# Kernel tuning notes

Measured on AMD Instinct MI355X. Metric: run time of the kernel, lower is better.

Reference implementation:

```python
import jax, jax.numpy as jnp
import numpy as np
import math

EPS = 1e-5
NEG_SLOPE = 0.2

def _patches(x, k=3, s=2):
    # x: (N, C, H, W) -> (N, C, k*k, Ho, Wo); VALID padding, stride s
    N, C = x.shape[0], x.shape[1]
    p = jax.lax.conv_general_dilated_patches(x, (k, k), (s, s), 'VALID')
    return p.reshape(N, C, k * k, p.shape[2], p.shape[3])

def _pacconv(x, guide, w, b, k=3):
    # PacConv2d (gaussian kernel, smooth_kernel_type='none', no normalization)
    xp = _patches(x)                              # (N,Cin,K2,Ho,Wo)
    gp = _patches(guide)                          # (N,Cg,K2,Ho,Wo)
    ctr = (k * k) // 2
    d = gp - gp[:, :, ctr:ctr + 1]
    ker = jnp.exp(-0.5 * jnp.sum(d * d, axis=1, keepdims=True))  # (N,1,K2,Ho,Wo)
    out = jnp.einsum('nckhw,ock->nohw', xp * ker,
                     w.reshape(w.shape[0], w.shape[1], k * k))
    return out + b[None, :, None, None]

def _conv(x, w, b):
    out = jax.lax.conv_general_dilated(x, w, (2, 2), 'VALID',
                                       dimension_numbers=('NCHW', 'OIHW', 'NCHW'))
    return out + b[None, :, None, None]

def _avgpool(x):
    s = jax.lax.reduce_window(x, 0.0, jax.lax.add, (1, 1, 3, 3), (1, 1, 2, 2), 'VALID')
    return s / 9.0

def _lrelu(x):
    return jnp.where(x >= 0, x, NEG_SLOPE * x)

def _bn(x, g, b):
    # training-mode BatchNorm2d (batch stats, biased variance)
    m = jnp.mean(x, axis=(0, 2, 3), keepdims=True)
    v = jnp.mean((x - m) ** 2, axis=(0, 2, 3), keepdims=True)
    xn = (x - m) * jax.lax.rsqrt(v + EPS)
    return xn * g[None, :, None, None] + b[None, :, None, None]

def setup_inputs() -> dict:
    key = jax.random.key(0)
    ks = jax.random.split(key, 12)
    N, Cin, H = 128, 1, 120
    x = jax.random.normal(ks[0], (N, Cin, H, H), jnp.float32)
    guide = jax.random.uniform(ks[1], (N, 1, H, H), jnp.float32)
    def wconv(k, co, ci):
        return jax.random.normal(k, (co, ci, 3, 3), jnp.float32) * (1.0 / math.sqrt(ci * 9))
    w1, b1 = wconv(ks[2], 32, Cin), jnp.zeros((32,), jnp.float32)
    w2, b2 = wconv(ks[3], 64, 32), jnp.zeros((64,), jnp.float32)
    w3, b3 = wconv(ks[4], 128, 64), jnp.zeros((128,), jnp.float32)
    w4, b4 = wconv(ks[5], 256, 128), jnp.zeros((256,), jnp.float32)
    g2, be2 = jnp.ones((64,), jnp.float32), jnp.zeros((64,), jnp.float32)
    g3, be3 = jnp.ones((128,), jnp.float32), jnp.zeros((128,), jnp.float32)
    g4, be4 = jnp.ones((256,), jnp.float32), jnp.zeros((256,), jnp.float32)
    wadv = jax.random.normal(ks[6], (1, 9216), jnp.float32)  # EqualLinear raw weight
    badv = jnp.ones((1,), jnp.float32)                        # bias_init=1
    return {"x": x, "guide": guide, "w1": w1, "b1": b1, "w2": w2, "b2": b2,
            "w3": w3, "b3": b3, "w4": w4, "b4": b4, "g2": g2, "be2": be2,
            "g3": g3, "be3": be3, "g4": g4, "be4": be4, "wadv": wadv, "badv": badv}

def reference(x, guide, w1, b1, w2, b2, w3, b3, w4, b4,
              g2, be2, g3, be3, g4, be4, wadv, badv):
    out = _lrelu(_conv(x, w1, b1))                 # (N,32,59,59)
    guide = _avgpool(guide)                        # (N,1,59,59)
    out = _bn(_lrelu(_pacconv(out, guide, w2, b2)), g2, be2)   # (N,64,29,29)
    guide = _avgpool(guide)                        # (N,1,29,29)
    out = _bn(_lrelu(_pacconv(out, guide, w3, b3)), g3, be3)   # (N,128,14,14)
    guide = _avgpool(guide)                        # (N,1,14,14)
    out = _bn(_lrelu(_pacconv(out, guide, w4, b4)), g4, be4)   # (N,256,6,6)
    flat = out.reshape(out.shape[0], -1)           # (N,9216)
    scale = 1.0 / math.sqrt(9216)
    validity = flat @ (wadv * scale).T + badv      # EqualLinear, lr_mul=1
    return validity
```

## Files before the change

kernel.cpp:

```cpp
#include <hip/hip_runtime.h>
#include <hip/hip_bf16.h>

#define EPSBN 1e-5f
#define NEG_SLOPE 0.2f

using f32x4  = __attribute__((ext_vector_type(4))) float;
using bf16x8 = __attribute__((ext_vector_type(8))) short;

#define O_Y1B     0
#define O_G1      7129088
#define O_Y2B     7574656
#define O_G2      11019392
#define O_WKB2    11127040
#define O_WKB3    11136256
#define O_WKB4    11173120
#define O_WADVR   11320576
#define O_ACC     11329792
#define O_G3      11336960
#define O_Y3B     11362048
#define O_POUT4   12967680
#define O_Y4      16506624
#define A_ACC2    0
#define A_ACC3    1024
#define A_ACC4    3072

__device__ __forceinline__ unsigned short f2bf(float f) {
  union { float f; unsigned int u; } v; v.f = f;
  unsigned int u = v.u + 0x7FFF + ((v.u >> 16) & 1);
  return (unsigned short)(u >> 16);
}
__device__ __forceinline__ float bf2f(unsigned short u) {
  union { unsigned int i; float f; } x; x.i = (unsigned int)u << 16; return x.f;
}

#define CONV1_B 7552
#define AVG1_B  1741
#define RPK_B   1548
#define ZERO_B  7
__global__ __launch_bounds__(256) void prep_kernel(
    const float* __restrict__ x, const float* __restrict__ gd,
    const float* __restrict__ w1, const float* __restrict__ b1,
    const float* __restrict__ w2, const float* __restrict__ w3,
    const float* __restrict__ w4, const float* __restrict__ wadv,
    float* __restrict__ ws) {
  const int bi = blockIdx.x, tid = threadIdx.x;
  __shared__ float xs[360];
  __shared__ float wsm[320];
  if (bi < CONV1_B) {
    const int n = bi / 59, oh = bi % 59;
    for (int i = tid; i < 320; i += 256)
      wsm[i] = (i < 288) ? w1[(i & 31) * 9 + (i >> 5)] : b1[i - 288];
    const float* src = x + ((size_t)n * 120 + oh * 2) * 120;
    for (int i = tid; i < 360; i += 256) xs[i] = src[i];
    __syncthreads();
    const int co = tid & 31;
    const int ow0 = (tid >> 5) * 8;
    float w[9];
#pragma unroll
    for (int k = 0; k < 9; ++k) w[k] = wsm[k * 32 + co];
    const float bias = wsm[288 + co];
    unsigned short* yb = (unsigned short*)(ws + O_Y1B) + (size_t)(n * 59 + oh) * 59 * 32;
#pragma unroll
    for (int j = 0; j < 8; ++j) {
      int ow = ow0 + j;
      if (ow < 59) {
        float acc = bias;
#pragma unroll
        for (int kh = 0; kh < 3; ++kh)
#pragma unroll
          for (int kw = 0; kw < 3; ++kw)
            acc += xs[kh * 120 + ow * 2 + kw] * w[kh * 3 + kw];
        acc = acc >= 0.0f ? acc : NEG_SLOPE * acc;
        yb[ow * 32 + co] = f2bf(acc);
      }
    }
  } else if (bi < CONV1_B + AVG1_B) {
    int idx = (bi - CONV1_B) * 256 + tid;
    if (idx < 445568) {
      int ow = idx % 59; int t = idx / 59; int oh = t % 59; int n = t / 59;
      const float* gb = gd + (n * 120 + oh * 2) * 120 + ow * 2;
      float s = 0.0f;
#pragma unroll
      for (int kh = 0; kh < 3; ++kh)
#pragma unroll
        for (int kw = 0; kw < 3; ++kw) s += gb[kh * 120 + kw];
      ws[O_G1 + idx] = s * (1.0f / 9.0f);
    }
  } else if (bi < CONV1_B + AVG1_B + RPK_B) {
    int idx = (bi - CONV1_B - AVG1_B) * 256 + tid;
    if (idx < 18432) {
      int kk = idx & 31; int t = idx >> 5; int co = t & 63; int tap = t >> 6;
      ((unsigned short*)(ws + O_WKB2))[idx] = f2bf(w2[(co * 32 + kk) * 9 + tap]);
    } else if (idx < 92160) {
      int i = idx - 18432;
      int kk = i & 31; int t = i >> 5; int co = t & 127; int t3 = t >> 7;
      int kc = t3 & 1; int tap = t3 >> 1;
      ((unsigned short*)(ws + O_WKB3))[i] = f2bf(w3[(co * 64 + kc * 32 + kk) * 9 + tap]);
    } else if (idx < 387072) {
      int i = idx - 92160;
      int kk = i & 31; int t = i >> 5; int co = t & 255; int t3 = t >> 8;
      int kc = t3 & 3; int tap = t3 >> 2;
      ((unsigned short*)(ws + O_WKB4))[i] = f2bf(w4[(co * 128 + kc * 32 + kk) * 9 + tap]);
    } else if (idx < 396288) {
      int i = idx - 387072;
      int c = i & 255; int hw = i >> 8;
      ws[O_WADVR + i] = wadv[c * 36 + hw] * (1.0f / 96.0f);
    }
  } else {
    int idx = (bi - CONV1_B - AVG1_B - RPK_B) * 256 + tid;
    if (idx * 4 < 7168) {
      float4 z = {0.0f, 0.0f, 0.0f, 0.0f};
      *reinterpret_cast<float4*>(ws + O_ACC + idx * 4) = z;
    }
  }
}

template <int CI, int CO, int HI, int HO, int NWM, int NWN, bool BN_IN,
          bool FUSE, int SSEG, int NBLK, int MINW, bool POOL>
__global__ __launch_bounds__(256, MINW)
void pac_kernel(const unsigned short* __restrict__ xb, const float* __restrict__ g,
                const float* __restrict__ wkb_f, const float* __restrict__ b,
                const float* __restrict__ gamma, const float* __restrict__ beta,
                const float* __restrict__ accin, float invM,
                unsigned short* __restrict__ yb, float* __restrict__ pout,
                float* __restrict__ accout,
                const float* __restrict__ pin, float* __restrict__ pgout,
                int PHI, int PHO, int PTOT) {
  constexpr int KC   = CI / 32;
  constexpr int NSEG = (9 * KC) / SSEG;
  constexpr int TSEG = SSEG / KC;
  static_assert(SSEG % KC == 0, "tap-aligned segments");
  constexpr int MBLK = NWM * 32;
  constexpr int PIX  = NBLK * MBLK;
  constexpr int BSZ  = BN_IN ? CI : 1;
  constexpr int PSM  = FUSE ? NWM : 1;
  constexpr int PSN  = FUSE ? CO * 2 : 1;
  const unsigned short* wkb = (const unsigned short*)wkb_f;

  const int tid  = threadIdx.x;
  const int bi   = blockIdx.x;

  if constexpr (POOL) {
    if (bi >= NBLK * NSEG) {
      int idx = (bi - NBLK * NSEG) * 256 + tid;
      if (idx < PTOT) {
        int ow = idx % PHO; int t = idx / PHO; int oh = t % PHO; int n = t / PHO;
        const float* gb = pin + (n * PHI + oh * 2) * PHI + ow * 2;
        float s = 0.0f;
#pragma unroll
        for (int kh = 0; kh < 3; ++kh)
#pragma unroll
          for (int kw = 0; kw < 3; ++kw) s += gb[kh * PHI + kw];
        pgout[idx] = s * (1.0f / 9.0f);
      }
      return;
    }
  }

  __shared__ float bscl[BSZ], bshl[BSZ];
  __shared__ float ps[PSM][PSN];

  const int lane = tid & 63;
  const int wv   = tid >> 6;
  const int wm   = wv / NWN, wn = wv % NWN;
  const int kseg = bi / NBLK;
  const int blk  = bi % NBLK;
  const int s0   = kseg * SSEG;
  const int tapb = kseg * TSEG;
  const int l15  = lane & 15;
  const int g8   = (lane >> 4) * 8;

  if constexpr (BN_IN) {
    if (tid < CI) {
      float s = 0.0f, q = 0.0f;
#pragma unroll
      for (int sl = 0; sl < 8; ++sl) {
        s += accin[(sl * CI + tid) * 2 + 0];
        q += accin[(sl * CI + tid) * 2 + 1];
      }
      float m = s * invM;
      float var = q * invM - m * m;
      float sc = gamma[tid] * rsqrtf(var + EPSBN);
      bscl[tid] = sc;
      bshl[tid] = beta[tid] - m * sc;
    }
    __syncthreads();
  }

  float kk[2][TSEG];
  int   xo[2];
  int   xt[TSEG];
#pragma unroll
  for (int t = 0; t < TSEG; ++t) {
    int tap = tapb + t;
    xt[t] = ((tap / 3) * HI + (tap % 3)) * CI;
  }
#pragma unroll
  for (int mt = 0; mt < 2; ++mt) {
    int p  = blk * MBLK + wm * 32 + mt * 16 + l15;
    int ow = p % HO, oh = (p / HO) % HO, n = p / (HO * HO);
    const float* gn = g + n * (HI * HI);
    float gc = gn[(oh * 2 + 1) * HI + ow * 2 + 1];
#pragma unroll
    for (int t = 0; t < TSEG; ++t) {
      int tap = tapb + t;
      float d = gn[(oh * 2 + tap / 3) * HI + ow * 2 + (tap % 3)] - gc;
      kk[mt][t] = __expf(-0.5f * d * d);
    }
    xo[mt] = ((n * HI + oh * 2) * HI + ow * 2) * CI;
  }

  f32x4 acc[2][4];
#pragma unroll
  for (int nt = 0; nt < 4; ++nt) {
    float bv = FUSE ? b[wn * 64 + nt * 16 + l15] : 0.0f;
#pragma unroll
    for (int mt = 0; mt < 2; ++mt) acc[mt][nt] = (f32x4){bv, bv, bv, bv};
  }

#pragma unroll
  for (int i = 0; i < SSEG; ++i) {
    const int t  = i / KC;
    const int kc = i % KC;
    bf16x8 bfv[4];
#pragma unroll
    for (int nt = 0; nt < 4; ++nt)
      bfv[nt] = *(const bf16x8*)(wkb + ((size_t)(s0 + i) * CO + wn * 64 + nt * 16 + l15) * 32 + g8);
    bf16x8 af[2];
#pragma unroll
    for (int mt = 0; mt < 2; ++mt) {
      const unsigned short* ax = xb + xo[mt] + xt[t] + kc * 32 + g8;
      bf16x8 u = *(const bf16x8*)ax;
      float v[8];
#pragma unroll
      for (int j = 0; j < 8; ++j) v[j] = bf2f((unsigned short)u[j]);
      if constexpr (BN_IN) {
        const int c0 = kc * 32 + g8;
#pragma unroll
        for (int j = 0; j < 8; ++j) v[j] = v[j] * bscl[c0 + j] + bshl[c0 + j];
      }
      const float kv = kk[mt][t];
#pragma unroll
      for (int j = 0; j < 8; ++j) v[j] *= kv;
#pragma unroll
      for (int j = 0; j < 8; ++j) af[mt][j] = (short)f2bf(v[j]);
    }
#pragma unroll
    for (int mt = 0; mt < 2; ++mt)
#pragma unroll
      for (int nt = 0; nt < 4; ++nt)
        acc[mt][nt] = __builtin_amdgcn_mfma_f32_16x16x32_bf16(af[mt], bfv[nt], acc[mt][nt], 0, 0, 0);
  }

  if constexpr (FUSE) {
#pragma unroll
    for (int nt = 0; nt < 4; ++nt) {
      const int co = wn * 64 + nt * 16 + l15;
      float s = 0.0f, q = 0.0f;
#pragma unroll
      for (int mt = 0; mt < 2; ++mt)
#pragma unroll
        for (int r = 0; r < 4; ++r) {
          float v = acc[mt][nt][r];
          v = v >= 0.0f ? v : NEG_SLOPE * v;
          int p = blk * MBLK + wm * 32 + mt * 16 + ((lane >> 4) << 2) + r;
          yb[(size_t)p * CO + co] = f2bf(v);
          s += v; q += v * v;
        }
      s += __shfl_xor(s, 16, 64); q += __shfl_xor(q, 16, 64);
      s += __shfl_xor(s, 32, 64); q += __shfl_xor(q, 32, 64);
      if (l15 == lane) { ps[wm][co * 2 + 0] = s; ps[wm][co * 2 + 1] = q; }
    }
    __syncthreads();
    if (tid < CO) {
      float s = 0.0f, q = 0.0f;
#pragma unroll
      for (int wmx = 0; wmx < NWM; ++wmx) { s += ps[wmx][tid * 2]; q += ps[wmx][tid * 2 + 1]; }
      atomicAdd(&accout[((blk & 7) * CO + tid) * 2 + 0], s);
      atomicAdd(&accout[((blk & 7) * CO + tid) * 2 + 1], q);
    }
  } else {
#pragma unroll
    for (int nt = 0; nt < 4; ++nt) {
      const int co = wn * 64 + nt * 16 + l15;
#pragma unroll
      for (int mt = 0; mt < 2; ++mt)
#pragma unroll
        for (int r = 0; r < 4; ++r) {
          int p = blk * MBLK + wm * 32 + mt * 16 + ((lane >> 4) << 2) + r;
          pout[((size_t)kseg * PIX + p) * CO + co] = acc[mt][nt][r];
        }
    }
  }
}

template <int CO, int EPT, int NSEG>
__global__ void combine_kernel(const float* __restrict__ pout, int pixco,
                               const float* __restrict__ b,
                               float* __restrict__ y, float* __restrict__ acc) {
  const int tid = threadIdx.x, blk = blockIdx.x;
  const int base = blk * (256 * EPT);
  const int co = tid & (CO - 1);
  const float bias = b[co];
  float s = 0.0f, q = 0.0f;
#pragma unroll
  for (int i = 0; i < EPT; ++i) {
    int e = base + i * 256 + tid;
    float v = bias;
#pragma unroll
    for (int sg = 0; sg < NSEG; ++sg) v += pout[(size_t)sg * pixco + e];
    v = v >= 0.0f ? v : NEG_SLOPE * v;
    y[e] = v;
    s += v; q += v * v;
  }
  atomicAdd(&acc[((blk & 7) * CO + co) * 2 + 0], s);
  atomicAdd(&acc[((blk & 7) * CO + co) * 2 + 1], q);
}

__global__ void linear_kernel(const float* __restrict__ y4, const float* __restrict__ acc4,
                              const float* __restrict__ bg4, const float* __restrict__ bb4,
                              const float* __restrict__ wadvr, const float* __restrict__ badv,
                              float* __restrict__ out) {
  int n = blockIdx.x, t = threadIdx.x;
  float s0 = 0.0f, q0 = 0.0f;
#pragma unroll
  for (int sl = 0; sl < 8; ++sl) {
    s0 += acc4[(sl * 256 + t) * 2 + 0];
    q0 += acc4[(sl * 256 + t) * 2 + 1];
  }
  float m = s0 * (1.0f / 4608.0f);
  float var = q0 * (1.0f / 4608.0f) - m * m;
  float sc = bg4[t] * rsqrtf(var + EPSBN);
  float sh = bb4[t] - m * sc;
  float s = 0.0f;
  for (int j = t; j < 9216; j += 256) s += (y4[n * 9216 + j] * sc + sh) * wadvr[j];
  __shared__ float ss[256];
  ss[t] = s; __syncthreads();
  for (int off = 128; off > 0; off >>= 1) {
    if (t < off) ss[t] += ss[t + off];
    __syncthreads();
  }
  if (t == 0) out[n] = ss[0] + badv[0];
}

extern "C" void kernel_launch(void* const* d_in, const int* in_sizes, int n_in,
                              void* d_out, int out_size, void* d_ws, size_t ws_size,
                              hipStream_t stream) {
  const float* x    = (const float*)d_in[0];
  const float* gd   = (const float*)d_in[1];
  const float* w1   = (const float*)d_in[2];
  const float* b1   = (const float*)d_in[3];
  const float* w2   = (const float*)d_in[4];
  const float* b2   = (const float*)d_in[5];
  const float* w3   = (const float*)d_in[6];
  const float* b3   = (const float*)d_in[7];
  const float* w4   = (const float*)d_in[8];
  const float* b4   = (const float*)d_in[9];
  const float* bg2  = (const float*)d_in[10];
  const float* bb2  = (const float*)d_in[11];
  const float* bg3  = (const float*)d_in[12];
  const float* bb3  = (const float*)d_in[13];
  const float* bg4  = (const float*)d_in[14];
  const float* bb4  = (const float*)d_in[15];
  const float* wadv = (const float*)d_in[16];
  const float* badv = (const float*)d_in[17];
  float* out = (float*)d_out;
  float* ws  = (float*)d_ws;

  unsigned short* y1b = (unsigned short*)(ws + O_Y1B);
  unsigned short* y2b = (unsigned short*)(ws + O_Y2B);
  unsigned short* y3b = (unsigned short*)(ws + O_Y3B);
  float* acc2 = ws + O_ACC + A_ACC2;
  float* acc3 = ws + O_ACC + A_ACC3;
  float* acc4 = ws + O_ACC + A_ACC4;

  prep_kernel<<<CONV1_B + AVG1_B + RPK_B + ZERO_B, 256, 0, stream>>>(
      x, gd, w1, b1, w2, w3, w4, wadv, ws);

  pac_kernel<32, 64, 59, 29, 4, 1, false, true, 9, 841, 3, true>
      <<<1262, 256, 0, stream>>>(y1b, ws + O_G1, ws + O_WKB2, b2,
                                 nullptr, nullptr, nullptr, 0.0f,
                                 y2b, nullptr, acc2,
                                 ws + O_G1, ws + O_G2, 59, 29, 107648);

  pac_kernel<64, 128, 29, 14, 2, 2, true, true, 18, 392, 2, true>
      <<<490, 256, 0, stream>>>(y2b, ws + O_G2, ws + O_WKB3, b3,
                                bg2, bb2, acc2, 1.0f / 107648.0f,
                                y3b, nullptr, acc3,
                                ws + O_G2, ws + O_G3, 29, 14, 25088);

  pac_kernel<128, 256, 14, 6, 1, 4, true, false, 12, 144, 2, false>
      <<<432, 256, 0, stream>>>(y3b, ws + O_G3, ws + O_WKB4, nullptr,
                                bg3, bb3, acc3, 1.0f / 25088.0f,
                                nullptr, ws + O_POUT4, nullptr,
                                nullptr, nullptr, 0, 0, 0);

  combine_kernel<256, 8, 3><<<576, 256, 0, stream>>>(ws + O_POUT4, 1179648, b4,
                                                     ws + O_Y4, acc4);

  linear_kernel<<<128, 256, 0, stream>>>(ws + O_Y4, acc4, bg4, bb4,
                                         ws + O_WADVR, badv, out);
}
```

Baseline: 105.4 us.

## Drop split-K for layer 4, fuse combine into pac kernel, stage stores through LDS

Removes the split-K segmentation so each pac block computes all taps. Layer 4 now applies bias, LeakyReLU and BN statistics in-kernel and writes bf16 output, so the combine kernel and its fp32 partial-sum round trip go away. Output tiles in both conv1 and the pac kernels are staged in shared memory and written with wide coalesced stores. The catch is that layer 4 launches only 144 blocks, each with a longer serial K loop, which lowers parallelism on a large GPU. f2bf now uses the HIP intrinsic, and linear_kernel reads bf16 activations.

```diff
diff --git a/kernel.cpp b/kernel.cpp
--- a/kernel.cpp
+++ b/kernel.cpp
@@ -18,16 +18,15 @@
 #define O_ACC     11329792
 #define O_G3      11336960
 #define O_Y3B     11362048
-#define O_POUT4   12967680
-#define O_Y4      16506624
+#define O_Y4B     12967680
 #define A_ACC2    0
 #define A_ACC3    1024
 #define A_ACC4    3072
 
 __device__ __forceinline__ unsigned short f2bf(float f) {
-  union { float f; unsigned int u; } v; v.f = f;
-  unsigned int u = v.u + 0x7FFF + ((v.u >> 16) & 1);
-  return (unsigned short)(u >> 16);
+  union { __hip_bfloat16 b; unsigned short u; } cv;
+  cv.b = __float2bfloat16(f);
+  return cv.u;
 }
 __device__ __forceinline__ float bf2f(unsigned short u) {
   union { unsigned int i; float f; } x; x.i = (unsigned int)u << 16; return x.f;
@@ -46,6 +45,7 @@
   const int bi = blockIdx.x, tid = threadIdx.x;
   __shared__ float xs[360];
   __shared__ float wsm[320];
+  __shared__ unsigned short ysm[1888];
   if (bi < CONV1_B) {
     const int n = bi / 59, oh = bi % 59;
     for (int i = tid; i < 320; i += 256)
@@ -59,7 +59,6 @@
 #pragma unroll
     for (int k = 0; k < 9; ++k) w[k] = wsm[k * 32 + co];
     const float bias = wsm[288 + co];
-    unsigned short* yb = (unsigned short*)(ws + O_Y1B) + (size_t)(n * 59 + oh) * 59 * 32;
 #pragma unroll
     for (int j = 0; j < 8; ++j) {
       int ow = ow0 + j;
@@ -71,9 +70,14 @@
           for (int kw = 0; kw < 3; ++kw)
             acc += xs[kh * 120 + ow * 2 + kw] * w[kh * 3 + kw];
         acc = acc >= 0.0f ? acc : NEG_SLOPE * acc;
-        yb[ow * 32 + co] = f2bf(acc);
-      }
-    }
+        ysm[ow * 32 + co] = f2bf(acc);
+      }
+    }
+    __syncthreads();
+    unsigned int* dst = (unsigned int*)((unsigned short*)(ws + O_Y1B) +
+                                        (size_t)(n * 59 + oh) * 1888);
+    const unsigned int* s2 = (const unsigned int*)ysm;
+    for (int i = tid; i < 944; i += 256) dst[i] = s2[i];
   } else if (bi < CONV1_B + AVG1_B) {
     int idx = (bi - CONV1_B) * 256 + tid;
     if (idx < 445568) {
@@ -116,33 +120,27 @@
 }
 
 template <int CI, int CO, int HI, int HO, int NWM, int NWN, bool BN_IN,
-          bool FUSE, int SSEG, int NBLK, int MINW, bool POOL>
+          int NBLK, int MINW, bool POOL>
 __global__ __launch_bounds__(256, MINW)
 void pac_kernel(const unsigned short* __restrict__ xb, const float* __restrict__ g,
                 const float* __restrict__ wkb_f, const float* __restrict__ b,
                 const float* __restrict__ gamma, const float* __restrict__ beta,
                 const float* __restrict__ accin, float invM,
-                unsigned short* __restrict__ yb, float* __restrict__ pout,
-                float* __restrict__ accout,
+                unsigned short* __restrict__ yb, float* __restrict__ accout,
                 const float* __restrict__ pin, float* __restrict__ pgout,
                 int PHI, int PHO, int PTOT) {
   constexpr int KC   = CI / 32;
-  constexpr int NSEG = (9 * KC) / SSEG;
-  constexpr int TSEG = SSEG / KC;
-  static_assert(SSEG % KC == 0, "tap-aligned segments");
+  constexpr int S    = 9 * KC;
   constexpr int MBLK = NWM * 32;
-  constexpr int PIX  = NBLK * MBLK;
   constexpr int BSZ  = BN_IN ? CI : 1;
-  constexpr int PSM  = FUSE ? NWM : 1;
-  constexpr int PSN  = FUSE ? CO * 2 : 1;
   const unsigned short* wkb = (const unsigned short*)wkb_f;
 
-  const int tid  = threadIdx.x;
-  const int bi   = blockIdx.x;
+  const int tid = threadIdx.x;
+  const int bi  = blockIdx.x;
 
   if constexpr (POOL) {
-    if (bi >= NBLK * NSEG) {
-      int idx = (bi - NBLK * NSEG) * 256 + tid;
+    if (bi >= NBLK) {
+      int idx = (bi - NBLK) * 256 + tid;
       if (idx < PTOT) {
         int ow = idx % PHO; int t = idx / PHO; int oh = t % PHO; int n = t / PHO;
         const float* gb = pin + (n * PHI + oh * 2) * PHI + ow * 2;
@@ -158,15 +156,13 @@
   }
 
   __shared__ float bscl[BSZ], bshl[BSZ];
-  __shared__ float ps[PSM][PSN];
+  __shared__ float ps[NWM][CO * 2];
+  __shared__ unsigned short ytile[4][2048];
 
   const int lane = tid & 63;
   const int wv   = tid >> 6;
   const int wm   = wv / NWN, wn = wv % NWN;
-  const int kseg = bi / NBLK;
-  const int blk  = bi % NBLK;
-  const int s0   = kseg * SSEG;
-  const int tapb = kseg * TSEG;
+  const int blk  = bi;
   const int l15  = lane & 15;
   const int g8   = (lane >> 4) * 8;
 
@@ -187,14 +183,8 @@
     __syncthreads();
   }
 
-  float kk[2][TSEG];
+  float kk[2][9];
   int   xo[2];
-  int   xt[TSEG];
-#pragma unroll
-  for (int t = 0; t < TSEG; ++t) {
-    int tap = tapb + t;
-    xt[t] = ((tap / 3) * HI + (tap % 3)) * CI;
-  }
 #pragma unroll
   for (int mt = 0; mt < 2; ++mt) {
     int p  = blk * MBLK + wm * 32 + mt * 16 + l15;
@@ -202,9 +192,8 @@
     const float* gn = g + n * (HI * HI);
     float gc = gn[(oh * 2 + 1) * HI + ow * 2 + 1];
 #pragma unroll
-    for (int t = 0; t < TSEG; ++t) {
-      int tap = tapb + t;
-      float d = gn[(oh * 2 + tap / 3) * HI + ow * 2 + (tap % 3)] - gc;
+    for (int t = 0; t < 9; ++t) {
+      float d = gn[(oh * 2 + t / 3) * HI + ow * 2 + (t % 3)] - gc;
       kk[mt][t] = __expf(-0.5f * d * d);
     }
     xo[mt] = ((n * HI + oh * 2) * HI + ow * 2) * CI;
@@ -213,24 +202,24 @@
   f32x4 acc[2][4];
 #pragma unroll
   for (int nt = 0; nt < 4; ++nt) {
-    float bv = FUSE ? b[wn * 64 + nt * 16 + l15] : 0.0f;
+    float bv = b[wn * 64 + nt * 16 + l15];
 #pragma unroll
     for (int mt = 0; mt < 2; ++mt) acc[mt][nt] = (f32x4){bv, bv, bv, bv};
   }
 
 #pragma unroll
-  for (int i = 0; i < SSEG; ++i) {
+  for (int i = 0; i < S; ++i) {
     const int t  = i / KC;
     const int kc = i % KC;
+    const int xoff = ((t / 3) * HI + (t % 3)) * CI + kc * 32 + g8;
     bf16x8 bfv[4];
 #pragma unroll
     for (int nt = 0; nt < 4; ++nt)
-      bfv[nt] = *(const bf16x8*)(wkb + ((size_t)(s0 + i) * CO + wn * 64 + nt * 16 + l15) * 32 + g8);
+      bfv[nt] = *(const bf16x8*)(wkb + ((size_t)i * CO + wn * 64 + nt * 16 + l15) * 32 + g8);
     bf16x8 af[2];
 #pragma unroll
     for (int mt = 0; mt < 2; ++mt) {
-      const unsigned short* ax = xb + xo[mt] + xt[t] + kc * 32 + g8;
-      bf16x8 u = *(const bf16x8*)ax;
+      bf16x8 u = *(const bf16x8*)(xb + xo[mt] + xoff);
       float v[8];
 #pragma unroll
       for (int j = 0; j < 8; ++j) v[j] = bf2f((unsigned short)u[j]);
@@ -252,72 +241,46 @@
         acc[mt][nt] = __builtin_amdgcn_mfma_f32_16x16x32_bf16(af[mt], bfv[nt], acc[mt][nt], 0, 0, 0);
   }
 
-  if constexpr (FUSE) {
-#pragma unroll
-    for (int nt = 0; nt < 4; ++nt) {
-      const int co = wn * 64 + nt * 16 + l15;
-      float s = 0.0f, q = 0.0f;
-#pragma unroll
-      for (int mt = 0; mt < 2; ++mt)
-#pragma unroll
-        for (int r = 0; r < 4; ++r) {
-          float v = acc[mt][nt][r];
-          v = v >= 0.0f ? v : NEG_SLOPE * v;
-          int p = blk * MBLK + wm * 32 + mt * 16 + ((lane >> 4) << 2) + r;
-          yb[(size_t)p * CO + co] = f2bf(v);
-          s += v; q += v * v;
-        }
-      s += __shfl_xor(s, 16, 64); q += __shfl_xor(q, 16, 64);
-      s += __shfl_xor(s, 32, 64); q += __shfl_xor(q, 32, 64);
-      if (l15 == lane) { ps[wm][co * 2 + 0] = s; ps[wm][co * 2 + 1] = q; }
-    }
-    __syncthreads();
-    if (tid < CO) {
-      float s = 0.0f, q = 0.0f;
-#pragma unroll
-      for (int wmx = 0; wmx < NWM; ++wmx) { s += ps[wmx][tid * 2]; q += ps[wmx][tid * 2 + 1]; }
-      atomicAdd(&accout[((blk & 7) * CO + tid) * 2 + 0], s);
-      atomicAdd(&accout[((blk & 7) * CO + tid) * 2 + 1], q);
-    }
-  } else {
-#pragma unroll
-    for (int nt = 0; nt < 4; ++nt) {
-      const int co = wn * 64 + nt * 16 + l15;
-#pragma unroll
-      for (int mt = 0; mt < 2; ++mt)
-#pragma unroll
-        for (int r = 0; r < 4; ++r) {
-          int p = blk * MBLK + wm * 32 + mt * 16 + ((lane >> 4) << 2) + r;
-          pout[((size_t)kseg * PIX + p) * CO + co] = acc[mt][nt][r];
-        }
-    }
-  }
-}
-
-template <int CO, int EPT, int NSEG>
-__global__ void combine_kernel(const float* __restrict__ pout, int pixco,
-                               const float* __restrict__ b,
-                               float* __restrict__ y, float* __restrict__ acc) {
-  const int tid = threadIdx.x, blk = blockIdx.x;
-  const int base = blk * (256 * EPT);
-  const int co = tid & (CO - 1);
-  const float bias = b[co];
-  float s = 0.0f, q = 0.0f;
-#pragma unroll
-  for (int i = 0; i < EPT; ++i) {
-    int e = base + i * 256 + tid;
-    float v = bias;
-#pragma unroll
-    for (int sg = 0; sg < NSEG; ++sg) v += pout[(size_t)sg * pixco + e];
-    v = v >= 0.0f ? v : NEG_SLOPE * v;
-    y[e] = v;
-    s += v; q += v * v;
-  }
-  atomicAdd(&acc[((blk & 7) * CO + co) * 2 + 0], s);
-  atomicAdd(&acc[((blk & 7) * CO + co) * 2 + 1], q);
-}
-
-__global__ void linear_kernel(const float* __restrict__ y4, const float* __restrict__ acc4,
+#pragma unroll
+  for (int nt = 0; nt < 4; ++nt) {
+    const int co = wn * 64 + nt * 16 + l15;
+    float s = 0.0f, q = 0.0f;
+#pragma unroll
+    for (int mt = 0; mt < 2; ++mt)
+#pragma unroll
+      for (int r = 0; r < 4; ++r) {
+        float v = acc[mt][nt][r];
+        v = v >= 0.0f ? v : NEG_SLOPE * v;
+        int row = mt * 16 + ((lane >> 4) << 2) + r;
+        ytile[wv][row * 64 + nt * 16 + l15] = f2bf(v);
+        s += v; q += v * v;
+      }
+    s += __shfl_xor(s, 16, 64); q += __shfl_xor(q, 16, 64);
+    s += __shfl_xor(s, 32, 64); q += __shfl_xor(q, 32, 64);
+    if (l15 == lane) { ps[wm][co * 2 + 0] = s; ps[wm][co * 2 + 1] = q; }
+  }
+  __syncthreads();
+  {
+    unsigned short* dbase = yb + (size_t)(blk * MBLK + wm * 32) * CO + wn * 64;
+    const uint4* srcT = (const uint4*)ytile[wv];
+#pragma unroll
+    for (int i = 0; i < 4; ++i) {
+      int row = i * 8 + (lane >> 3);
+      int u4  = lane & 7;
+      *(uint4*)(dbase + (size_t)row * CO + u4 * 8) = srcT[row * 8 + u4];
+    }
+  }
+  if (tid < CO) {
+    float s = 0.0f, q = 0.0f;
+#pragma unroll
+    for (int wmx = 0; wmx < NWM; ++wmx) { s += ps[wmx][tid * 2]; q += ps[wmx][tid * 2 + 1]; }
+    atomicAdd(&accout[((blk & 7) * CO + tid) * 2 + 0], s);
+    atomicAdd(&accout[((blk & 7) * CO + tid) * 2 + 1], q);
+  }
+}
+
+__global__ void linear_kernel(const unsigned short* __restrict__ y4b,
+                              const float* __restrict__ acc4,
                               const float* __restrict__ bg4, const float* __restrict__ bb4,
                               const float* __restrict__ wadvr, const float* __restrict__ badv,
                               float* __restrict__ out) {
@@ -333,7 +296,8 @@
   float sc = bg4[t] * rsqrtf(var + EPSBN);
   float sh = bb4[t] - m * sc;
   float s = 0.0f;
-  for (int j = t; j < 9216; j += 256) s += (y4[n * 9216 + j] * sc + sh) * wadvr[j];
+  for (int j = t; j < 9216; j += 256)
+    s += (bf2f(y4b[n * 9216 + j]) * sc + sh) * wadvr[j];
   __shared__ float ss[256];
   ss[t] = s; __syncthreads();
   for (int off = 128; off > 0; off >>= 1) {
@@ -370,6 +334,7 @@
   unsigned short* y1b = (unsigned short*)(ws + O_Y1B);
   unsigned short* y2b = (unsigned short*)(ws + O_Y2B);
   unsigned short* y3b = (unsigned short*)(ws + O_Y3B);
+  unsigned short* y4b = (unsigned short*)(ws + O_Y4B);
   float* acc2 = ws + O_ACC + A_ACC2;
   float* acc3 = ws + O_ACC + A_ACC3;
   float* acc4 = ws + O_ACC + A_ACC4;
@@ -377,27 +342,24 @@
   prep_kernel<<<CONV1_B + AVG1_B + RPK_B + ZERO_B, 256, 0, stream>>>(
       x, gd, w1, b1, w2, w3, w4, wadv, ws);
 
-  pac_kernel<32, 64, 59, 29, 4, 1, false, true, 9, 841, 3, true>
+  pac_kernel<32, 64, 59, 29, 4, 1, false, 841, 3, true>
       <<<1262, 256, 0, stream>>>(y1b, ws + O_G1, ws + O_WKB2, b2,
                                  nullptr, nullptr, nullptr, 0.0f,
-                                 y2b, nullptr, acc2,
+                                 y2b, acc2,
                                  ws + O_G1, ws + O_G2, 59, 29, 107648);
 
-  pac_kernel<64, 128, 29, 14, 2, 2, true, true, 18, 392, 2, true>
+  pac_kernel<64, 128, 29, 14, 2, 2, true, 392, 2, true>
       <<<490, 256, 0, stream>>>(y2b, ws + O_G2, ws + O_WKB3, b3,
                                 bg2, bb2, acc2, 1.0f / 107648.0f,
-                                y3b, nullptr, acc3,
+                                y3b, acc3,
                                 ws + O_G2, ws + O_G3, 29, 14, 25088);
 
-  pac_kernel<128, 256, 14, 6, 1, 4, true, false, 12, 144, 2, false>
-      <<<432, 256, 0, stream>>>(y3b, ws + O_G3, ws + O_WKB4, nullptr,
+  pac_kernel<128, 256, 14, 6, 1, 4, true, 144, 2, false>
+      <<<144, 256, 0, stream>>>(y3b, ws + O_G3, ws + O_WKB4, b4,
                                 bg3, bb3, acc3, 1.0f / 25088.0f,
-                                nullptr, ws + O_POUT4, nullptr,
+                                y4b, acc4,
                                 nullptr, nullptr, 0, 0, 0);
 
-  combine_kernel<256, 8, 3><<<576, 256, 0, stream>>>(ws + O_POUT4, 1179648, b4,
-                                                     ws + O_Y4, acc4);
-
-  linear_kernel<<<128, 256, 0, stream>>>(ws + O_Y4, acc4, bg4, bb4,
+  linear_kernel<<<128, 256, 0, stream>>>(y4b, acc4, bg4, bb4,
                                          ws + O_WADVR, badv, out);
 }
```

Measured after the change: 105.4 us. No clear change (+0.0%).
